# Performance work log

Measured on AMD Instinct MI355X. Metric: run time of the kernel, lower is better.

## Reference

```python
import jax, jax.numpy as jnp
import numpy as np

N_HEADS = 16


def setup_inputs() -> dict:
    key = jax.random.key(0)
    k1, k2, k3 = jax.random.split(key, 3)
    B, T, D = 4, 2048, 1024
    x = jax.random.normal(k1, (B, T, D), dtype=jnp.float32)
    # weights stored as (in, out); equivalent to torch Linear weight.T
    w_qkv = jax.random.normal(k2, (D, 3 * D), dtype=jnp.float32) * (D ** -0.5)
    w_proj = jax.random.normal(k3, (D, D), dtype=jnp.float32) * (D ** -0.5)
    b_proj = jnp.zeros((D,), dtype=jnp.float32)
    return {"x": x, "w_qkv": w_qkv, "w_proj": w_proj, "b_proj": b_proj}


def reference(x, w_qkv, w_proj, b_proj):
    B, T, D = x.shape
    H = N_HEADS
    Dh = D // H
    scale = Dh ** -0.5
    qkv = x @ w_qkv                                  # (B, T, 3D)
    qkv = qkv.reshape(B, T, 3, H, Dh)
    q, k, v = (jnp.transpose(qkv[:, :, i], (0, 2, 1, 3)) for i in range(3))  # (B,H,T,Dh)
    attn = jnp.einsum('bhqd,bhkd->bhqk', q, k) * scale  # (B,H,T,T)
    causal_mask = jnp.triu(jnp.ones((T, T), dtype=bool), k=1)
    attn = jnp.where(causal_mask, -jnp.inf, attn)
    attn = jax.nn.softmax(attn, axis=-1)
    out = jnp.einsum('bhqk,bhkd->bhqd', attn, v)     # (B,H,T,Dh)
    out = jnp.transpose(out, (0, 2, 1, 3)).reshape(B, T, D)
    return out @ w_proj + b_proj
```

## Files before the change

### kernel.cpp

```cpp
#include <hip/hip_runtime.h>
#include <hip/hip_bf16.h>
#include <stdint.h>
#include <stddef.h>

typedef __bf16 bf16_t;
typedef __bf16 bf16x4 __attribute__((ext_vector_type(4)));
typedef __bf16 bf16x8 __attribute__((ext_vector_type(8)));
typedef float  f32x4  __attribute__((ext_vector_type(4)));

static __device__ __forceinline__ f32x4 zero4() { return (f32x4){0.f, 0.f, 0.f, 0.f}; }

#define MFMA16(a, b, c) __builtin_amdgcn_mfma_f32_16x16x32_bf16((a), (b), (c), 0, 0, 0)

#define GLOAD_LDS16(gptr, lptr)                                                        \
  __builtin_amdgcn_global_load_lds((const __attribute__((address_space(1))) void*)(gptr), \
                                   (__attribute__((address_space(3))) void*)(lptr), 16, 0, 0)

__global__ __launch_bounds__(256) void k_cast(const float* __restrict__ in,
                                              bf16_t* __restrict__ out) {
  size_t i = (size_t)blockIdx.x * 256 + threadIdx.x;
  const float4* p = (const float4*)in;
  float4 a = p[i * 2 + 0];
  float4 b = p[i * 2 + 1];
  bf16x8 v;
  v[0] = (bf16_t)a.x; v[1] = (bf16_t)a.y; v[2] = (bf16_t)a.z; v[3] = (bf16_t)a.w;
  v[4] = (bf16_t)b.x; v[5] = (bf16_t)b.y; v[6] = (bf16_t)b.z; v[7] = (bf16_t)b.w;
  *(bf16x8*)(out + i * 8) = v;
}

__global__ __launch_bounds__(256) void k_tcast(const float* __restrict__ in,
                                               bf16_t* __restrict__ out,
                                               int R, int C) {
  __shared__ bf16_t tile[64][72];
  int c0 = blockIdx.x * 64, r0 = blockIdx.y * 64;
  int t = threadIdx.x;
  int r = t >> 2, cc = (t & 3) * 16;
  const float* src = in + (size_t)(r0 + r) * C + c0 + cc;
#pragma unroll
  for (int q = 0; q < 4; ++q) {
    float4 v = *(const float4*)(src + q * 4);
    tile[r][cc + q * 4 + 0] = (bf16_t)v.x;
    tile[r][cc + q * 4 + 1] = (bf16_t)v.y;
    tile[r][cc + q * 4 + 2] = (bf16_t)v.z;
    tile[r][cc + q * 4 + 3] = (bf16_t)v.w;
  }
  __syncthreads();
  int c = t >> 2, rr = (t & 3) * 16;
  bf16x8 o0, o1;
#pragma unroll
  for (int j = 0; j < 8; ++j) { o0[j] = tile[rr + j][c]; o1[j] = tile[rr + 8 + j][c]; }
  bf16_t* dst = out + (size_t)(c0 + c) * R + r0 + rr;
  *(bf16x8*)dst = o0;
  *(bf16x8*)(dst + 8) = o1;
}

__global__ __launch_bounds__(256) void k_vtrans(const bf16_t* __restrict__ qkv,
                                                bf16_t* __restrict__ vT) {
  __shared__ bf16_t tile[64][72];
  int t0 = blockIdx.x * 64, bh = blockIdx.y;
  int b = bh >> 4, h = bh & 15;
  int t = threadIdx.x;
  int tr = t >> 2, cc = (t & 3) * 16;
  const bf16_t* src = qkv + (size_t)(b * 2048 + t0 + tr) * 3072 + 2048 + h * 64 + cc;
  bf16x8 a0 = *(const bf16x8*)src;
  bf16x8 a1 = *(const bf16x8*)(src + 8);
#pragma unroll
  for (int j = 0; j < 8; ++j) { tile[tr][cc + j] = a0[j]; tile[tr][cc + 8 + j] = a1[j]; }
  __syncthreads();
  int d = t >> 2, tt = (t & 3) * 16;
  bf16x8 o0, o1;
#pragma unroll
  for (int j = 0; j < 8; ++j) { o0[j] = tile[tt + j][d]; o1[j] = tile[tt + 8 + j][d]; }
  bf16_t* dst = vT + (size_t)(bh * 64 + d) * 2048 + t0 + tt;
  *(bf16x8*)dst = o0;
  *(bf16x8*)(dst + 8) = o1;
}

__global__ __launch_bounds__(256) void k_kprep(const bf16_t* __restrict__ qkv,
                                               bf16_t* __restrict__ kh) {
  int t0 = blockIdx.x * 64, bh = blockIdx.y;
  int b = bh >> 4, h = bh & 15;
  int t = threadIdx.x;
  int r = t >> 2, c = (t & 3) * 16;
  const bf16_t* src = qkv + (size_t)(b * 2048 + t0 + r) * 3072 + 1024 + h * 64 + c;
  bf16x8 a0 = *(const bf16x8*)src;
  bf16x8 a1 = *(const bf16x8*)(src + 8);
#pragma unroll
  for (int j = 0; j < 8; ++j) {
    a0[j] = (bf16_t)(0.18033688011f * (float)a0[j]);
    a1[j] = (bf16_t)(0.18033688011f * (float)a1[j]);
  }
  bf16_t* dst = kh + ((size_t)bh * 2048 + t0 + r) * 64 + c;
  *(bf16x8*)dst = a0;
  *(bf16x8*)(dst + 8) = a1;
}

template <bool BF16OUT>
__global__ __launch_bounds__(256) void k_gemm_bt(const bf16_t* __restrict__ A,
                                                 const bf16_t* __restrict__ BT,
                                                 void* __restrict__ Cout,
                                                 const float* __restrict__ bias,
                                                 int M, int N, int K) {
  __shared__ bf16_t sA[128 * 32];
  __shared__ bf16_t sB[128 * 32];
  int tid = threadIdx.x;
  int wid = tid >> 6, lane = tid & 63;
  int cl = lane & 15, gp = lane >> 4;
  int nwg = gridDim.x * gridDim.y;
  int flat = blockIdx.y * gridDim.x + blockIdx.x;
  int cpx = nwg >> 3;
  int swzid = (flat & 7) * cpx + (flat >> 3);
  int brow = (swzid / gridDim.x) * 128, bcol = (swzid % gridDim.x) * 128;
  int wr = wid >> 1, wc = wid & 1;
  f32x4 acc[4][4];
#pragma unroll
  for (int i = 0; i < 4; ++i)
#pragma unroll
    for (int j = 0; j < 4; ++j) acc[i][j] = zero4();

  int srow = tid >> 2;
  int sk = (tid & 3) * 8;
  const bf16_t* gA = A + (size_t)(brow + srow) * K + sk;
  const bf16_t* gB = BT + (size_t)(bcol + srow) * K + sk;
  char* lA = (char*)sA + wid * 1024;
  char* lB = (char*)sB + wid * 1024;

  for (int k0 = 0; k0 < K; k0 += 32) {
    __syncthreads();
    GLOAD_LDS16(gA + k0, lA);
    GLOAD_LDS16(gA + (size_t)64 * K + k0, lA + 4096);
    GLOAD_LDS16(gB + k0, lB);
    GLOAD_LDS16(gB + (size_t)64 * K + k0, lB + 4096);
    __syncthreads();
    bf16x8 af[4], bfr[4];
#pragma unroll
    for (int i = 0; i < 4; ++i)
      af[i] = *(const bf16x8*)&sA[(wr * 64 + i * 16 + cl) * 32 + gp * 8];
#pragma unroll
    for (int j = 0; j < 4; ++j)
      bfr[j] = *(const bf16x8*)&sB[(wc * 64 + j * 16 + cl) * 32 + gp * 8];
#pragma unroll
    for (int i = 0; i < 4; ++i)
#pragma unroll
      for (int j = 0; j < 4; ++j)
        acc[i][j] = MFMA16(af[i], bfr[j], acc[i][j]);
  }

#pragma unroll
  for (int i = 0; i < 4; ++i) {
    int row0 = brow + wr * 64 + i * 16 + gp * 4;
#pragma unroll
    for (int j = 0; j < 4; ++j) {
      int col = bcol + wc * 64 + j * 16 + cl;
#pragma unroll
      for (int e = 0; e < 4; ++e) {
        size_t idx = (size_t)(row0 + e) * N + col;
        if (BF16OUT)
          ((bf16_t*)Cout)[idx] = (bf16_t)acc[i][j][e];
        else
          ((float*)Cout)[idx] = acc[i][j][e] + bias[col];
      }
    }
  }
}

static __device__ __forceinline__ void softmax16(f32x4 (&s)[4], f32x4 (&o)[4],
                                                 float& mrun, float& lsum, char* Pw,
                                                 int kv0, int qw, int swz, int cl, int gp) {
  if (kv0 + 63 > qw) {
    int thr = qw + cl - kv0 - gp * 4;
#pragma unroll
    for (int jj = 0; jj < 4; ++jj)
#pragma unroll
      for (int e = 0; e < 4; ++e)
        if (jj * 16 + e > thr) s[jj][e] = -1e30f;
  }
  float pm01 = fmaxf(fmaxf(fmaxf(s[0][0], s[0][1]), fmaxf(s[0][2], s[0][3])),
                     fmaxf(fmaxf(s[1][0], s[1][1]), fmaxf(s[1][2], s[1][3])));
  float pm23 = fmaxf(fmaxf(fmaxf(s[2][0], s[2][1]), fmaxf(s[2][2], s[2][3])),
                     fmaxf(fmaxf(s[3][0], s[3][1]), fmaxf(s[3][2], s[3][3])));
  float pm = fmaxf(pm01, pm23);
  pm = fmaxf(pm, __shfl_xor(pm, 16));
  pm = fmaxf(pm, __shfl_xor(pm, 32));
  float mnew = mrun;
  if (!__all(pm <= mnew + 11.5f)) {
    float mold = mnew;
    mnew = fmaxf(mold, pm);
    float aa = exp2f(mold - mnew);
    mrun = mnew;
    lsum *= aa;
#pragma unroll
    for (int e = 0; e < 4; ++e) {
      float ae = __shfl(aa, gp * 4 + e);
#pragma unroll
      for (int c = 0; c < 4; ++c) o[c][e] *= ae;
    }
  }
  float rsj[4];
#pragma unroll
  for (int jj = 0; jj < 4; ++jj) {
    float p0 = exp2f(s[jj][0] - mnew);
    float p1 = exp2f(s[jj][1] - mnew);
    float p2 = exp2f(s[jj][2] - mnew);
    float p3 = exp2f(s[jj][3] - mnew);
    rsj[jj] = (p0 + p1) + (p2 + p3);
    bf16x4 pw;
    pw[0] = (bf16_t)p0; pw[1] = (bf16_t)p1; pw[2] = (bf16_t)p2; pw[3] = (bf16_t)p3;
    *(bf16x4*)(Pw + cl * 128 + ((jj * 32 + gp * 8) ^ swz)) = pw;
  }
  float rs = (rsj[0] + rsj[1]) + (rsj[2] + rsj[3]);
  rs += __shfl_xor(rs, 16);
  rs += __shfl_xor(rs, 32);
  lsum += rs;
}

static __device__ __forceinline__ void pass16(const char* __restrict__ bK,
                                              const char* __restrict__ bV,
                                              char* __restrict__ Pw,
                                              const bf16x8& qa, const bf16x8& qb,
                                              f32x4 (&o)[4], float& mrun, float& lsum,
                                              int kv0, int qw, int swz, int cl, int gp) {
  f32x4 s[4];
#pragma unroll
  for (int jj = 0; jj < 4; ++jj) {
    const char* base = bK + (jj * 16 + cl) * 128;
    bf16x8 k0 = *(const bf16x8*)(base + ((gp * 16) ^ swz));
    bf16x8 k1 = *(const bf16x8*)(base + ((64 + gp * 16) ^ swz));
    f32x4 a = zero4();
    a = MFMA16(k0, qa, a);
    a = MFMA16(k1, qb, a);
    s[jj] = a;
  }
  softmax16(s, o, mrun, lsum, Pw, kv0, qw, swz, cl, gp);

  asm volatile("" ::: "memory");
  bf16x8 pa0 = *(const bf16x8*)(Pw + cl * 128 + ((gp * 16) ^ swz));
  bf16x8 pa1 = *(const bf16x8*)(Pw + cl * 128 + ((64 + gp * 16) ^ swz));

  __builtin_amdgcn_s_setprio(1);
#pragma unroll
  for (int c = 0; c < 4; ++c) {
    const char* base = bV + (c * 16 + cl) * 128;
    bf16x8 v0 = *(const bf16x8*)(base + ((gp * 16) ^ swz));
    bf16x8 v1 = *(const bf16x8*)(base + ((64 + gp * 16) ^ swz));
    o[c] = MFMA16(pa0, v0, o[c]);
    o[c] = MFMA16(pa1, v1, o[c]);
  }
  __builtin_amdgcn_s_setprio(0);
  asm volatile("" ::: "memory");
}

__global__ __launch_bounds__(256, 4) void k_attn5(const bf16_t* __restrict__ qkv,
                                                  const bf16_t* __restrict__ kh,
                                                  const bf16_t* __restrict__ vT,
                                                  bf16_t* __restrict__ out) {
  __shared__ alignas(16) char sK[2][8192];
  __shared__ alignas(16) char sV[2][8192];
  __shared__ alignas(16) char sP[4][2048];

  int n = blockIdx.x;
  int bh = ((n & 7) << 3) | ((n >> 3) & 7);
  int pr = n >> 6;
  int jL = pr, jH = 31 - pr;
  int b = bh >> 4, h = bh & 15;
  int tid = threadIdx.x, wid = tid >> 6, lane = tid & 63;
  int cl = lane & 15, gp = lane >> 4;

  int qwL = jL * 64 + wid * 16;
  int qwH = jH * 64 + wid * 16;

  bf16x8 qL0, qL1, qH0, qH1;
  {
    const bf16_t* p = qkv + (size_t)(b * 2048 + qwL + cl) * 3072 + h * 64 + gp * 8;
    qL0 = *(const bf16x8*)p; qL1 = *(const bf16x8*)(p + 32);
    p = qkv + (size_t)(b * 2048 + qwH + cl) * 3072 + h * 64 + gp * 8;
    qH0 = *(const bf16x8*)p; qH1 = *(const bf16x8*)(p + 32);
  }

  int srow = tid >> 3;
  int swzcb = ((tid & 7) * 16) ^ ((srow & 7) << 4);
  const bf16_t* gK = kh + ((size_t)bh * 2048 + srow) * 64 + (swzcb >> 1);
  const bf16_t* gV = vT + ((size_t)(bh * 64) + srow) * 2048 + (swzcb >> 1);

  f32x4 oL[4], oH[4];
#pragma unroll
  for (int c = 0; c < 4; ++c) { oL[c] = zero4(); oH[c] = zero4(); }
  float mrunL = -1e30f, lsumL = 0.f, mrunH = -1e30f, lsumH = 0.f;

  int swz = (cl & 7) << 4;
  int nt = jH + 1;
  char* Pw = sP[wid];

  {
    char* lK = sK[0] + wid * 1024;
    char* lV = sV[0] + wid * 1024;
    GLOAD_LDS16(gK, lK);
    GLOAD_LDS16(gK + 32 * 64, lK + 4096);
    GLOAD_LDS16(gV, lV);
    GLOAD_LDS16(gV + (size_t)32 * 2048, lV + 4096);
  }
  asm volatile("s_waitcnt vmcnt(0)");
  __syncthreads();

  for (int t = 0; t < nt; ++t) {
    int cur = t & 1;
    int kv0 = t * 64;
    if (t + 1 < nt) {
      int kv1 = kv0 + 64;
      char* lK = sK[cur ^ 1] + wid * 1024;
      char* lV = sV[cur ^ 1] + wid * 1024;
      GLOAD_LDS16(gK + (size_t)kv1 * 64, lK);
      GLOAD_LDS16(gK + (size_t)(kv1 + 32) * 64, lK + 4096);
      GLOAD_LDS16(gV + kv1, lV);
      GLOAD_LDS16(gV + kv1 + (size_t)32 * 2048, lV + 4096);
    }
    const char* bK = sK[cur];
    const char* bV = sV[cur];

    if (t <= jL)
      pass16(bK, bV, Pw, qL0, qL1, oL, mrunL, lsumL, kv0, qwL, swz, cl, gp);
    pass16(bK, bV, Pw, qH0, qH1, oH, mrunH, lsumH, kv0, qwH, swz, cl, gp);

    asm volatile("s_waitcnt vmcnt(0)");
    __syncthreads();
  }

#pragma unroll
  for (int e = 0; e < 4; ++e) {
    float iL = 1.0f / __shfl(lsumL, gp * 4 + e);
    float iH = 1.0f / __shfl(lsumH, gp * 4 + e);
    int rL = qwL + gp * 4 + e;
    int rH = qwH + gp * 4 + e;
#pragma unroll
    for (int c = 0; c < 4; ++c) {
      int col = h * 64 + c * 16 + cl;
      out[(size_t)(b * 2048 + rL) * 1024 + col] = (bf16_t)(oL[c][e] * iL);
      out[(size_t)(b * 2048 + rH) * 1024 + col] = (bf16_t)(oH[c][e] * iH);
    }
  }
}

extern "C" void kernel_launch(void* const* d_in, const int* in_sizes, int n_in,
                              void* d_out, int out_size, void* d_ws, size_t ws_size,
                              hipStream_t stream) {
  const float* x      = (const float*)d_in[0];
  const float* w_qkv  = (const float*)d_in[1];
  const float* w_proj = (const float*)d_in[2];
  const float* b_proj = (const float*)d_in[3];
  float* outp = (float*)d_out;

  char* ws = (char*)d_ws;
  bf16_t* xb     = (bf16_t*)(ws);
  bf16_t* wqkvT  = (bf16_t*)(ws + 16777216);
  bf16_t* wprojT = (bf16_t*)(ws + 16777216 + 6291456);
  bf16_t* qkv    = (bf16_t*)(ws + 16777216 + 6291456 + 2097152);
  bf16_t* vT     = (bf16_t*)(ws + 16777216 + 6291456 + 2097152 + 50331648);
  bf16_t* aout   = (bf16_t*)(ws + 16777216 + 6291456 + 2097152 + 50331648 + 16777216);
  bf16_t* kh     = xb;

  k_cast<<<dim3(8192 * 1024 / (256 * 8)), 256, 0, stream>>>(x, xb);
  k_tcast<<<dim3(3072 / 64, 1024 / 64), 256, 0, stream>>>(w_qkv, wqkvT, 1024, 3072);
  k_tcast<<<dim3(1024 / 64, 1024 / 64), 256, 0, stream>>>(w_proj, wprojT, 1024, 1024);
  k_gemm_bt<true><<<dim3(3072 / 128, 8192 / 128), 256, 0, stream>>>(
      xb, wqkvT, (void*)qkv, nullptr, 8192, 3072, 1024);
  k_kprep<<<dim3(32, 64), 256, 0, stream>>>(qkv, kh);
  k_vtrans<<<dim3(32, 64), 256, 0, stream>>>(qkv, vT);
  k_attn5<<<dim3(1024), 256, 0, stream>>>(qkv, kh, vT, aout);
  k_gemm_bt<false><<<dim3(1024 / 128, 8192 / 128), 256, 0, stream>>>(
      aout, wprojT, (void*)outp, b_proj, 8192, 1024, 1024);
}
```

Before: 286.7 us.

## Fuse Q/K/V head-split, K scaling and V transpose into QKV GEMM epilogue

The QKV GEMM epilogue now writes Q and K directly in per-head layout, with the softmax scale folded into K, and transposes V through LDS into vT. This removes the separate kprep and vtrans kernels and the round-trip through the interleaved qkv buffer. The attention kernel also computes the softmax row sum with an MFMA against a ones vector instead of per-lane adds and shuffles, and raises wave priority during the QK MFMAs. The trade-offs are extra LDS (vtile) in the GEMM, which may reduce occupancy, strided epilogue stores, and extra MFMA work per tile in attention.

```diff
diff --git a/kernel.cpp b/kernel.cpp
--- a/kernel.cpp
+++ b/kernel.cpp
@@ -54,53 +54,99 @@
   *(bf16x8*)(dst + 8) = o1;
 }
 
-__global__ __launch_bounds__(256) void k_vtrans(const bf16_t* __restrict__ qkv,
-                                                bf16_t* __restrict__ vT) {
-  __shared__ bf16_t tile[64][72];
-  int t0 = blockIdx.x * 64, bh = blockIdx.y;
-  int b = bh >> 4, h = bh & 15;
-  int t = threadIdx.x;
-  int tr = t >> 2, cc = (t & 3) * 16;
-  const bf16_t* src = qkv + (size_t)(b * 2048 + t0 + tr) * 3072 + 2048 + h * 64 + cc;
-  bf16x8 a0 = *(const bf16x8*)src;
-  bf16x8 a1 = *(const bf16x8*)(src + 8);
-#pragma unroll
-  for (int j = 0; j < 8; ++j) { tile[tr][cc + j] = a0[j]; tile[tr][cc + 8 + j] = a1[j]; }
-  __syncthreads();
-  int d = t >> 2, tt = (t & 3) * 16;
-  bf16x8 o0, o1;
-#pragma unroll
-  for (int j = 0; j < 8; ++j) { o0[j] = tile[tt + j][d]; o1[j] = tile[tt + 8 + j][d]; }
-  bf16_t* dst = vT + (size_t)(bh * 64 + d) * 2048 + t0 + tt;
-  *(bf16x8*)dst = o0;
-  *(bf16x8*)(dst + 8) = o1;
-}
-
-__global__ __launch_bounds__(256) void k_kprep(const bf16_t* __restrict__ qkv,
-                                               bf16_t* __restrict__ kh) {
-  int t0 = blockIdx.x * 64, bh = blockIdx.y;
-  int b = bh >> 4, h = bh & 15;
-  int t = threadIdx.x;
-  int r = t >> 2, c = (t & 3) * 16;
-  const bf16_t* src = qkv + (size_t)(b * 2048 + t0 + r) * 3072 + 1024 + h * 64 + c;
-  bf16x8 a0 = *(const bf16x8*)src;
-  bf16x8 a1 = *(const bf16x8*)(src + 8);
-#pragma unroll
-  for (int j = 0; j < 8; ++j) {
-    a0[j] = (bf16_t)(0.18033688011f * (float)a0[j]);
-    a1[j] = (bf16_t)(0.18033688011f * (float)a1[j]);
-  }
-  bf16_t* dst = kh + ((size_t)bh * 2048 + t0 + r) * 64 + c;
-  *(bf16x8*)dst = a0;
-  *(bf16x8*)(dst + 8) = a1;
-}
-
-template <bool BF16OUT>
-__global__ __launch_bounds__(256) void k_gemm_bt(const bf16_t* __restrict__ A,
-                                                 const bf16_t* __restrict__ BT,
-                                                 void* __restrict__ Cout,
-                                                 const float* __restrict__ bias,
-                                                 int M, int N, int K) {
+__global__ __launch_bounds__(256) void k_gemm_qkv(const bf16_t* __restrict__ A,
+                                                  const bf16_t* __restrict__ BT,
+                                                  bf16_t* __restrict__ qh,
+                                                  bf16_t* __restrict__ kh,
+                                                  bf16_t* __restrict__ vT) {
+  constexpr int K = 1024;
+  __shared__ bf16_t sA[128 * 32];
+  __shared__ bf16_t sB[128 * 32];
+  __shared__ bf16_t vtile[4][64][72];
+  int tid = threadIdx.x;
+  int wid = tid >> 6, lane = tid & 63;
+  int cl = lane & 15, gp = lane >> 4;
+  int nwg = gridDim.x * gridDim.y;
+  int flat = blockIdx.y * gridDim.x + blockIdx.x;
+  int cpx = nwg >> 3;
+  int swzid = (flat & 7) * cpx + (flat >> 3);
+  int brow = (swzid / gridDim.x) * 128, bcol = (swzid % gridDim.x) * 128;
+  int wr = wid >> 1, wc = wid & 1;
+  f32x4 acc[4][4];
+#pragma unroll
+  for (int i = 0; i < 4; ++i)
+#pragma unroll
+    for (int j = 0; j < 4; ++j) acc[i][j] = zero4();
+
+  int srow = tid >> 2;
+  int sk = (tid & 3) * 8;
+  const bf16_t* gA = A + (size_t)(brow + srow) * K + sk;
+  const bf16_t* gB = BT + (size_t)(bcol + srow) * K + sk;
+  char* lA = (char*)sA + wid * 1024;
+  char* lB = (char*)sB + wid * 1024;
+
+  for (int k0 = 0; k0 < K; k0 += 32) {
+    __syncthreads();
+    GLOAD_LDS16(gA + k0, lA);
+    GLOAD_LDS16(gA + (size_t)64 * K + k0, lA + 4096);
+    GLOAD_LDS16(gB + k0, lB);
+    GLOAD_LDS16(gB + (size_t)64 * K + k0, lB + 4096);
+    __syncthreads();
+    bf16x8 af[4], bfr[4];
+#pragma unroll
+    for (int i = 0; i < 4; ++i)
+      af[i] = *(const bf16x8*)&sA[(wr * 64 + i * 16 + cl) * 32 + gp * 8];
+#pragma unroll
+    for (int j = 0; j < 4; ++j)
+      bfr[j] = *(const bf16x8*)&sB[(wc * 64 + j * 16 + cl) * 32 + gp * 8];
+#pragma unroll
+    for (int i = 0; i < 4; ++i)
+#pragma unroll
+      for (int j = 0; j < 4; ++j)
+        acc[i][j] = MFMA16(af[i], bfr[j], acc[i][j]);
+  }
+
+  int b_ = brow >> 11;
+  int t0 = (brow & 2047) + wr * 64;
+  int colbase = bcol + wc * 64;
+  int region = colbase >> 10;
+  int h_ = (colbase & 1023) >> 6;
+  size_t bh_ = (size_t)(b_ * 16 + h_);
+
+  if (region < 2) {
+    bf16_t* dst = (region == 0 ? qh : kh) + (bh_ * 2048 + t0) * 64;
+    float sc = (region == 0) ? 1.0f : 0.18033688011f;
+#pragma unroll
+    for (int i = 0; i < 4; ++i)
+#pragma unroll
+      for (int j = 0; j < 4; ++j)
+#pragma unroll
+        for (int e = 0; e < 4; ++e)
+          dst[(size_t)(i * 16 + gp * 4 + e) * 64 + j * 16 + cl] =
+              (bf16_t)(acc[i][j][e] * sc);
+  } else {
+    bf16_t (*vt)[72] = vtile[wid];
+#pragma unroll
+    for (int i = 0; i < 4; ++i)
+#pragma unroll
+      for (int j = 0; j < 4; ++j)
+#pragma unroll
+        for (int e = 0; e < 4; ++e)
+          vt[j * 16 + cl][i * 16 + gp * 4 + e] = (bf16_t)acc[i][j][e];
+    int d = lane;
+    const bf16_t* src = &vt[d][0];
+    bf16_t* dst = vT + (bh_ * 64 + d) * 2048 + t0;
+#pragma unroll
+    for (int tt = 0; tt < 64; tt += 8)
+      *(bf16x8*)(dst + tt) = *(const bf16x8*)(src + tt);
+  }
+}
+
+__global__ __launch_bounds__(256) void k_gemm_proj(const bf16_t* __restrict__ A,
+                                                   const bf16_t* __restrict__ BT,
+                                                   float* __restrict__ Cout,
+                                                   const float* __restrict__ bias,
+                                                   int M, int N, int K) {
   __shared__ bf16_t sA[128 * 32];
   __shared__ bf16_t sB[128 * 32];
   int tid = threadIdx.x;
@@ -153,20 +199,33 @@
     for (int j = 0; j < 4; ++j) {
       int col = bcol + wc * 64 + j * 16 + cl;
 #pragma unroll
-      for (int e = 0; e < 4; ++e) {
-        size_t idx = (size_t)(row0 + e) * N + col;
-        if (BF16OUT)
-          ((bf16_t*)Cout)[idx] = (bf16_t)acc[i][j][e];
-        else
-          ((float*)Cout)[idx] = acc[i][j][e] + bias[col];
-      }
+      for (int e = 0; e < 4; ++e)
+        Cout[(size_t)(row0 + e) * N + col] = acc[i][j][e] + bias[col];
     }
   }
 }
 
-static __device__ __forceinline__ void softmax16(f32x4 (&s)[4], f32x4 (&o)[4],
-                                                 float& mrun, float& lsum, char* Pw,
-                                                 int kv0, int qw, int swz, int cl, int gp) {
+static __device__ __forceinline__ void pass16(const char* __restrict__ bK,
+                                              const char* __restrict__ bV,
+                                              char* __restrict__ Pw,
+                                              const bf16x8& qa, const bf16x8& qb,
+                                              const bf16x8& ones8,
+                                              f32x4 (&o)[4], f32x4& ol, float& mrun,
+                                              int kv0, int qw, int swz, int cl, int gp) {
+  f32x4 s[4];
+  __builtin_amdgcn_s_setprio(1);
+#pragma unroll
+  for (int jj = 0; jj < 4; ++jj) {
+    const char* base = bK + (jj * 16 + cl) * 128;
+    bf16x8 k0 = *(const bf16x8*)(base + ((gp * 16) ^ swz));
+    bf16x8 k1 = *(const bf16x8*)(base + ((64 + gp * 16) ^ swz));
+    f32x4 a = zero4();
+    a = MFMA16(k0, qa, a);
+    a = MFMA16(k1, qb, a);
+    s[jj] = a;
+  }
+  __builtin_amdgcn_s_setprio(0);
+
   if (kv0 + 63 > qw) {
     int thr = qw + cl - kv0 - gp * 4;
 #pragma unroll
@@ -188,56 +247,29 @@
     mnew = fmaxf(mold, pm);
     float aa = exp2f(mold - mnew);
     mrun = mnew;
-    lsum *= aa;
 #pragma unroll
     for (int e = 0; e < 4; ++e) {
       float ae = __shfl(aa, gp * 4 + e);
+      ol[e] *= ae;
 #pragma unroll
       for (int c = 0; c < 4; ++c) o[c][e] *= ae;
     }
   }
-  float rsj[4];
 #pragma unroll
   for (int jj = 0; jj < 4; ++jj) {
-    float p0 = exp2f(s[jj][0] - mnew);
-    float p1 = exp2f(s[jj][1] - mnew);
-    float p2 = exp2f(s[jj][2] - mnew);
-    float p3 = exp2f(s[jj][3] - mnew);
-    rsj[jj] = (p0 + p1) + (p2 + p3);
     bf16x4 pw;
-    pw[0] = (bf16_t)p0; pw[1] = (bf16_t)p1; pw[2] = (bf16_t)p2; pw[3] = (bf16_t)p3;
+#pragma unroll
+    for (int e = 0; e < 4; ++e) pw[e] = (bf16_t)exp2f(s[jj][e] - mnew);
     *(bf16x4*)(Pw + cl * 128 + ((jj * 32 + gp * 8) ^ swz)) = pw;
   }
-  float rs = (rsj[0] + rsj[1]) + (rsj[2] + rsj[3]);
-  rs += __shfl_xor(rs, 16);
-  rs += __shfl_xor(rs, 32);
-  lsum += rs;
-}
-
-static __device__ __forceinline__ void pass16(const char* __restrict__ bK,
-                                              const char* __restrict__ bV,
-                                              char* __restrict__ Pw,
-                                              const bf16x8& qa, const bf16x8& qb,
-                                              f32x4 (&o)[4], float& mrun, float& lsum,
-                                              int kv0, int qw, int swz, int cl, int gp) {
-  f32x4 s[4];
-#pragma unroll
-  for (int jj = 0; jj < 4; ++jj) {
-    const char* base = bK + (jj * 16 + cl) * 128;
-    bf16x8 k0 = *(const bf16x8*)(base + ((gp * 16) ^ swz));
-    bf16x8 k1 = *(const bf16x8*)(base + ((64 + gp * 16) ^ swz));
-    f32x4 a = zero4();
-    a = MFMA16(k0, qa, a);
-    a = MFMA16(k1, qb, a);
-    s[jj] = a;
-  }
-  softmax16(s, o, mrun, lsum, Pw, kv0, qw, swz, cl, gp);
 
   asm volatile("" ::: "memory");
   bf16x8 pa0 = *(const bf16x8*)(Pw + cl * 128 + ((gp * 16) ^ swz));
   bf16x8 pa1 = *(const bf16x8*)(Pw + cl * 128 + ((64 + gp * 16) ^ swz));
 
   __builtin_amdgcn_s_setprio(1);
+  ol = MFMA16(pa0, ones8, ol);
+  ol = MFMA16(pa1, ones8, ol);
 #pragma unroll
   for (int c = 0; c < 4; ++c) {
     const char* base = bV + (c * 16 + cl) * 128;
@@ -250,7 +282,7 @@
   asm volatile("" ::: "memory");
 }
 
-__global__ __launch_bounds__(256, 4) void k_attn5(const bf16_t* __restrict__ qkv,
+__global__ __launch_bounds__(256, 4) void k_attn6(const bf16_t* __restrict__ qh,
                                                   const bf16_t* __restrict__ kh,
                                                   const bf16_t* __restrict__ vT,
                                                   bf16_t* __restrict__ out) {
@@ -262,7 +294,7 @@
   int bh = ((n & 7) << 3) | ((n >> 3) & 7);
   int pr = n >> 6;
   int jL = pr, jH = 31 - pr;
-  int b = bh >> 4, h = bh & 15;
+  int b = bh >> 4;
   int tid = threadIdx.x, wid = tid >> 6, lane = tid & 63;
   int cl = lane & 15, gp = lane >> 4;
 
@@ -271,21 +303,24 @@
 
   bf16x8 qL0, qL1, qH0, qH1;
   {
-    const bf16_t* p = qkv + (size_t)(b * 2048 + qwL + cl) * 3072 + h * 64 + gp * 8;
+    const bf16_t* p = qh + ((size_t)bh * 2048 + qwL + cl) * 64 + gp * 8;
     qL0 = *(const bf16x8*)p; qL1 = *(const bf16x8*)(p + 32);
-    p = qkv + (size_t)(b * 2048 + qwH + cl) * 3072 + h * 64 + gp * 8;
+    p = qh + ((size_t)bh * 2048 + qwH + cl) * 64 + gp * 8;
     qH0 = *(const bf16x8*)p; qH1 = *(const bf16x8*)(p + 32);
   }
+  bf16x8 ones8;
+#pragma unroll
+  for (int e = 0; e < 8; ++e) ones8[e] = (bf16_t)1.0f;
 
   int srow = tid >> 3;
   int swzcb = ((tid & 7) * 16) ^ ((srow & 7) << 4);
   const bf16_t* gK = kh + ((size_t)bh * 2048 + srow) * 64 + (swzcb >> 1);
   const bf16_t* gV = vT + ((size_t)(bh * 64) + srow) * 2048 + (swzcb >> 1);
 
-  f32x4 oL[4], oH[4];
+  f32x4 oL[4], oH[4], olL = zero4(), olH = zero4();
 #pragma unroll
   for (int c = 0; c < 4; ++c) { oL[c] = zero4(); oH[c] = zero4(); }
-  float mrunL = -1e30f, lsumL = 0.f, mrunH = -1e30f, lsumH = 0.f;
+  float mrunL = -1e30f, mrunH = -1e30f;
 
   int swz = (cl & 7) << 4;
   int nt = jH + 1;
@@ -318,8 +353,8 @@
     const char* bV = sV[cur];
 
     if (t <= jL)
-      pass16(bK, bV, Pw, qL0, qL1, oL, mrunL, lsumL, kv0, qwL, swz, cl, gp);
-    pass16(bK, bV, Pw, qH0, qH1, oH, mrunH, lsumH, kv0, qwH, swz, cl, gp);
+      pass16(bK, bV, Pw, qL0, qL1, ones8, oL, olL, mrunL, kv0, qwL, swz, cl, gp);
+    pass16(bK, bV, Pw, qH0, qH1, ones8, oH, olH, mrunH, kv0, qwH, swz, cl, gp);
 
     asm volatile("s_waitcnt vmcnt(0)");
     __syncthreads();
@@ -327,10 +362,11 @@
 
 #pragma unroll
   for (int e = 0; e < 4; ++e) {
-    float iL = 1.0f / __shfl(lsumL, gp * 4 + e);
-    float iH = 1.0f / __shfl(lsumH, gp * 4 + e);
+    float iL = 1.0f / olL[e];
+    float iH = 1.0f / olH[e];
     int rL = qwL + gp * 4 + e;
     int rH = qwH + gp * 4 + e;
+    int h = bh & 15;
 #pragma unroll
     for (int c = 0; c < 4; ++c) {
       int col = h * 64 + c * 16 + cl;
@@ -351,21 +387,18 @@
 
   char* ws = (char*)d_ws;
   bf16_t* xb     = (bf16_t*)(ws);
-  bf16_t* wqkvT  = (bf16_t*)(ws + 16777216);
-  bf16_t* wprojT = (bf16_t*)(ws + 16777216 + 6291456);
-  bf16_t* qkv    = (bf16_t*)(ws + 16777216 + 6291456 + 2097152);
-  bf16_t* vT     = (bf16_t*)(ws + 16777216 + 6291456 + 2097152 + 50331648);
-  bf16_t* aout   = (bf16_t*)(ws + 16777216 + 6291456 + 2097152 + 50331648 + 16777216);
-  bf16_t* kh     = xb;
+  bf16_t* wqkvT  = (bf16_t*)(ws + (16u << 20));
+  bf16_t* wprojT = (bf16_t*)(ws + (22u << 20));
+  bf16_t* qh     = (bf16_t*)(ws + (24u << 20));
+  bf16_t* kh     = (bf16_t*)(ws + (40u << 20));
+  bf16_t* vT     = (bf16_t*)(ws + (56u << 20));
+  bf16_t* aout   = (bf16_t*)(ws + (72u << 20));
 
   k_cast<<<dim3(8192 * 1024 / (256 * 8)), 256, 0, stream>>>(x, xb);
   k_tcast<<<dim3(3072 / 64, 1024 / 64), 256, 0, stream>>>(w_qkv, wqkvT, 1024, 3072);
   k_tcast<<<dim3(1024 / 64, 1024 / 64), 256, 0, stream>>>(w_proj, wprojT, 1024, 1024);
-  k_gemm_bt<true><<<dim3(3072 / 128, 8192 / 128), 256, 0, stream>>>(
-      xb, wqkvT, (void*)qkv, nullptr, 8192, 3072, 1024);
-  k_kprep<<<dim3(32, 64), 256, 0, stream>>>(qkv, kh);
-  k_vtrans<<<dim3(32, 64), 256, 0, stream>>>(qkv, vT);
-  k_attn5<<<dim3(1024), 256, 0, stream>>>(qkv, kh, vT, aout);
-  k_gemm_bt<false><<<dim3(1024 / 128, 8192 / 128), 256, 0, stream>>>(
-      aout, wprojT, (void*)outp, b_proj, 8192, 1024, 1024);
-}
+  k_gemm_qkv<<<dim3(3072 / 128, 8192 / 128), 256, 0, stream>>>(xb, wqkvT, qh, kh, vT);
+  k_attn6<<<dim3(1024), 256, 0, stream>>>(qh, kh, vT, aout);
+  k_gemm_proj<<<dim3(1024 / 128, 8192 / 128), 256, 0, stream>>>(
+      aout, wprojT, outp, b_proj, 8192, 1024, 1024);
+}
```

New measurement: 277.4 us. 3.2% less time.
